# Kernel tuning notes

Hardware: AMD Instinct MI355X
Metric: run time of the kernel (lower is better)

## Reference

```python
import jax, jax.numpy as jnp
import numpy as np

B, N, DIN, DOUT, H = 4, 2048, 256, 256, 4
HD = DOUT // H
NEG_SLOPE = 0.2


def setup_inputs() -> dict:
    key = jax.random.key(0)
    k1, k2, k3, k4, k5 = jax.random.split(key, 5)
    x = jax.random.normal(k1, (B, N, DIN), dtype=jnp.float32)
    adj = jax.random.randint(k2, (B, N, N), 0, 2).astype(jnp.float32)
    # ensure self-loops so every softmax row has at least one valid entry
    adj = jnp.maximum(adj, jnp.eye(N, dtype=jnp.float32)[None])
    # xavier-uniform-ish scales
    w_bound = float(np.sqrt(6.0 / (DIN + DOUT)))
    a_bound = float(np.sqrt(6.0 / (1 + HD)))
    W = jax.random.uniform(k3, (DOUT, DIN), jnp.float32, -w_bound, w_bound)
    a_src = jax.random.uniform(k4, (H, HD), jnp.float32, -a_bound, a_bound)
    a_dst = jax.random.uniform(k5, (H, HD), jnp.float32, -a_bound, a_bound)
    return {"x": x, "adj": adj, "W": W, "a_src": a_src, "a_dst": a_dst}


def reference(x, adj, W, a_src, a_dst):
    b, n, _ = x.shape
    h = (x @ W.T).reshape(b, n, H, HD)                      # [B,N,H,HD]
    s_src = jnp.einsum('bnhd,hd->bnh', h, a_src)            # [B,N,H]
    s_dst = jnp.einsum('bnhd,hd->bnh', h, a_dst)            # [B,N,H]
    # e[b,i,j,h] = leaky_relu(s_src[b,i,h] + s_dst[b,j,h])
    e = jax.nn.leaky_relu(s_src[:, :, None, :] + s_dst[:, None, :, :], NEG_SLOPE)
    e = jnp.where(adj[..., None] == 0, -jnp.inf, e)         # [B,N,N,H]
    alpha = jax.nn.softmax(e, axis=2)                       # softmax over j (dropout is identity at eval)
    out = jnp.einsum('bijh,bjhd->bihd', alpha, h)           # weighted aggregate
    return out.reshape(b, n, DOUT)
```

## Files before the change

### kernel.cpp

```cpp
#include <hip/hip_runtime.h>
#include <math.h>

#define Bb   4
#define Nn   2048
#define Dd   256
#define Hh   4
#define HDd  64

typedef float v4f __attribute__((ext_vector_type(4)));
typedef short v8s __attribute__((ext_vector_type(8)));

__device__ __forceinline__ unsigned rne_bf16(float f) {
    unsigned u = __float_as_uint(f);
    u += 0x7fffu + ((u >> 16) & 1u);
    return u >> 16;
}

__global__ __launch_bounds__(256, 2) void k_gemm(const float* __restrict__ x,
                                                 const float* __restrict__ W,
                                                 const float* __restrict__ a_src,
                                                 const float* __restrict__ a_dst,
                                                 unsigned short* __restrict__ hbf,
                                                 float* __restrict__ ssrc,
                                                 float* __restrict__ sdst) {
    __shared__ __align__(16) unsigned short xs[2][64 * 72];
    __shared__ __align__(16) unsigned short wsm[2][64 * 72];
    __shared__ float asd[128];

    const int tid = threadIdx.x;
    const int m0 = (int)(blockIdx.x >> 2) * 64;
    const int head = (int)blockIdx.x & 3;
    const int n0 = head * 64;
    const int b = m0 >> 11;
    const int i0loc = m0 & 2047;

    if (tid < 128) {
        int sel = tid >> 6, d = tid & 63;
        asd[tid] = sel ? a_dst[n0 + d] : a_src[n0 + d];
    }

    const int wv = tid >> 6, ln = tid & 63, l15 = ln & 15, l4 = ln >> 4;
    const int mh = wv >> 1, nh = wv & 1;
    const int srow = tid >> 2, kq = (tid & 3) * 16;

    v4f acc[2][2];
#pragma unroll
    for (int g = 0; g < 2; ++g)
#pragma unroll
        for (int t = 0; t < 2; ++t) acc[g][t] = (v4f){0.f, 0.f, 0.f, 0.f};

    for (int st = 0; st < 4; ++st) {
        const int k0 = st * 64;
        __syncthreads();
        {
            float xf[16], wf[16];
            const float* xp = x + (size_t)(m0 + srow) * Dd + k0 + kq;
            const float* wp = W + (size_t)(n0 + srow) * Dd + k0 + kq;
#pragma unroll
            for (int q = 0; q < 4; ++q) {
                *(float4*)&xf[q * 4] = *(const float4*)(xp + q * 4);
                *(float4*)&wf[q * 4] = *(const float4*)(wp + q * 4);
            }
            unsigned xh[8], xl[8], wh[8], wl[8];
#pragma unroll
            for (int j = 0; j < 8; ++j) {
                unsigned h0 = rne_bf16(xf[2 * j]), h1 = rne_bf16(xf[2 * j + 1]);
                float l0 = xf[2 * j] - __uint_as_float(h0 << 16);
                float l1 = xf[2 * j + 1] - __uint_as_float(h1 << 16);
                xh[j] = h0 | (h1 << 16);
                xl[j] = rne_bf16(l0) | (rne_bf16(l1) << 16);
                unsigned g0 = rne_bf16(wf[2 * j]), g1 = rne_bf16(wf[2 * j + 1]);
                float m0f = wf[2 * j] - __uint_as_float(g0 << 16);
                float m1f = wf[2 * j + 1] - __uint_as_float(g1 << 16);
                wh[j] = g0 | (g1 << 16);
                wl[j] = rne_bf16(m0f) | (rne_bf16(m1f) << 16);
            }
            *(uint4*)(xs[0] + srow * 72 + kq)     = make_uint4(xh[0], xh[1], xh[2], xh[3]);
            *(uint4*)(xs[0] + srow * 72 + kq + 8) = make_uint4(xh[4], xh[5], xh[6], xh[7]);
            *(uint4*)(xs[1] + srow * 72 + kq)     = make_uint4(xl[0], xl[1], xl[2], xl[3]);
            *(uint4*)(xs[1] + srow * 72 + kq + 8) = make_uint4(xl[4], xl[5], xl[6], xl[7]);
            *(uint4*)(wsm[0] + srow * 72 + kq)     = make_uint4(wh[0], wh[1], wh[2], wh[3]);
            *(uint4*)(wsm[0] + srow * 72 + kq + 8) = make_uint4(wh[4], wh[5], wh[6], wh[7]);
            *(uint4*)(wsm[1] + srow * 72 + kq)     = make_uint4(wl[0], wl[1], wl[2], wl[3]);
            *(uint4*)(wsm[1] + srow * 72 + kq + 8) = make_uint4(wl[4], wl[5], wl[6], wl[7]);
        }
        __syncthreads();
        {
            v8s ah[2][2], al[2][2], bh_[2][2], bl_[2][2];
#pragma unroll
            for (int g = 0; g < 2; ++g)
#pragma unroll
                for (int kh = 0; kh < 2; ++kh) {
                    int ro = (mh * 32 + g * 16 + l15) * 72 + kh * 32 + l4 * 8;
                    ah[g][kh] = *(const v8s*)(xs[0] + ro);
                    al[g][kh] = *(const v8s*)(xs[1] + ro);
                }
#pragma unroll
            for (int t = 0; t < 2; ++t)
#pragma unroll
                for (int kh = 0; kh < 2; ++kh) {
                    int ro = (nh * 32 + t * 16 + l15) * 72 + kh * 32 + l4 * 8;
                    bh_[t][kh] = *(const v8s*)(wsm[0] + ro);
                    bl_[t][kh] = *(const v8s*)(wsm[1] + ro);
                }
#pragma unroll
            for (int g = 0; g < 2; ++g)
#pragma unroll
                for (int t = 0; t < 2; ++t)
#pragma unroll
                    for (int kh = 0; kh < 2; ++kh) {
                        acc[g][t] = __builtin_amdgcn_mfma_f32_16x16x32_bf16(ah[g][kh], bh_[t][kh], acc[g][t], 0, 0, 0);
                        acc[g][t] = __builtin_amdgcn_mfma_f32_16x16x32_bf16(al[g][kh], bh_[t][kh], acc[g][t], 0, 0, 0);
                        acc[g][t] = __builtin_amdgcn_mfma_f32_16x16x32_bf16(ah[g][kh], bl_[t][kh], acc[g][t], 0, 0, 0);
                    }
        }
    }

    __syncthreads();
    float* T = (float*)&xs[0][0];
#pragma unroll
    for (int g = 0; g < 2; ++g)
#pragma unroll
        for (int t = 0; t < 2; ++t)
#pragma unroll
            for (int r = 0; r < 4; ++r) {
                int d = nh * 32 + t * 16 + l15;
                int m = mh * 32 + g * 16 + l4 * 4 + r;
                T[d * 67 + m] = acc[g][t][r];
            }
    __syncthreads();
    if (tid < 128) {
        int m = tid & 63, sel = tid >> 6;
        float s = 0.f;
#pragma unroll
        for (int d = 0; d < 64; ++d) s += T[d * 67 + m] * asd[sel * 64 + d];
        (sel ? sdst : ssrc)[((size_t)b * Nn + i0loc + m) * Hh + head] = s;
        int dloc = tid >> 1, jh = tid & 1;
        const float* row = T + dloc * 67 + jh * 32;
        unsigned pk[16];
#pragma unroll
        for (int jj = 0; jj < 16; ++jj)
            pk[jj] = rne_bf16(row[jj * 2]) | (rne_bf16(row[jj * 2 + 1]) << 16);
        unsigned short* dst = hbf +
            ((size_t)((b * 64 + (i0loc >> 5) + jh) * 256 + head * HDd + dloc)) * 32;
        uint4* d4 = (uint4*)dst;
        d4[0] = make_uint4(pk[0], pk[1], pk[2], pk[3]);
        d4[1] = make_uint4(pk[4], pk[5], pk[6], pk[7]);
        d4[2] = make_uint4(pk[8], pk[9], pk[10], pk[11]);
        d4[3] = make_uint4(pk[12], pk[13], pk[14], pk[15]);
    }
}

__global__ __launch_bounds__(512, 4) void k_aggr(const unsigned short* __restrict__ hbf,
                                                 const float* __restrict__ adj,
                                                 const float* __restrict__ ssrc,
                                                 const float* __restrict__ sdst,
                                                 float* __restrict__ out) {
    __shared__ __align__(16) unsigned short Bh[128 * 72];
    __shared__ __align__(16) unsigned short Aw[64 * 72];

    const int tid = threadIdx.x;
    const int bid = (int)blockIdx.x;
    const int hp  = (bid >> 3) & 1;
    const int lin = (bid & 7) | ((bid >> 4) << 3);
    const int b  = lin >> 6;
    const int i0 = (lin & 63) * 32;

    const int gi = tid >> 4, jq = tid & 15;
    const int srow = tid >> 2, sseg = tid & 3;
    const int wv = tid >> 6;
    const int hl = wv >> 2, tl = wv & 3;
    const int ln = tid & 63, l15 = ln & 15, l4 = ln >> 4;

    const float2 s2 = *(const float2*)(ssrc + ((size_t)b * Nn + i0 + gi) * Hh + hp * 2);
    const float* adjr = adj + (size_t)b * Nn * Nn + (size_t)(i0 + gi) * Nn;
    const float* sdr = sdst + (size_t)b * Nn * Hh + hp * 2;

    const v8s ones = {0x3F80, 0x3F80, 0x3F80, 0x3F80, 0x3F80, 0x3F80, 0x3F80, 0x3F80};

    v4f acc[2], zac[2];
#pragma unroll
    for (int g = 0; g < 2; ++g) {
        acc[g] = (v4f){0.f, 0.f, 0.f, 0.f};
        zac[g] = (v4f){0.f, 0.f, 0.f, 0.f};
    }

    for (int st = 0; st < 32; ++st) {
        const int j0 = st * 64;
        const uint4* src = (const uint4*)(hbf +
            ((size_t)((b * 64 + 2 * st + (sseg >> 1)) * 256 + hp * 128 + srow)) * 32 +
            (sseg & 1) * 16);
        uint4 p0 = src[0], p1 = src[1];
        float4 ajv = *(const float4*)(adjr + j0 + jq * 4);
        float2 sd0 = *(const float2*)(sdr + (size_t)(j0 + jq * 4 + 0) * Hh);
        float2 sd1 = *(const float2*)(sdr + (size_t)(j0 + jq * 4 + 1) * Hh);
        float2 sd2 = *(const float2*)(sdr + (size_t)(j0 + jq * 4 + 2) * Hh);
        float2 sd3 = *(const float2*)(sdr + (size_t)(j0 + jq * 4 + 3) * Hh);
        __syncthreads();
        {
            uint4* dh = (uint4*)(Bh + srow * 72 + sseg * 16);
            dh[0] = p0; dh[1] = p1;
        }
        {
            const float adjv[4] = {ajv.x, ajv.y, ajv.z, ajv.w};
            const float2 sdv[4] = {sd0, sd1, sd2, sd3};
            unsigned pk0[2], pk1[2];
#pragma unroll
            for (int k = 0; k < 4; ++k) {
                float e0 = s2.x + sdv[k].x;
                float e1 = s2.y + sdv[k].y;
                e0 = fmaxf(e0, 0.2f * e0);
                e1 = fmaxf(e1, 0.2f * e1);
                unsigned u0 = rne_bf16(adjv[k] * __expf(e0));
                unsigned u1 = rne_bf16(adjv[k] * __expf(e1));
                if (k & 1) { pk0[k >> 1] |= u0 << 16; pk1[k >> 1] |= u1 << 16; }
                else       { pk0[k >> 1] = u0;        pk1[k >> 1] = u1; }
            }
            *(uint2*)(Aw + (gi) * 72 + jq * 4)      = make_uint2(pk0[0], pk0[1]);
            *(uint2*)(Aw + (32 + gi) * 72 + jq * 4) = make_uint2(pk1[0], pk1[1]);
        }
        __syncthreads();
        {
            v8s a[2][2], bf[2];
#pragma unroll
            for (int g = 0; g < 2; ++g)
#pragma unroll
                for (int kh = 0; kh < 2; ++kh)
                    a[g][kh] = *(const v8s*)(Aw + (hl * 32 + g * 16 + l15) * 72 + kh * 32 + l4 * 8);
#pragma unroll
            for (int kh = 0; kh < 2; ++kh)
                bf[kh] = *(const v8s*)(Bh + (hl * 64 + tl * 16 + l15) * 72 + kh * 32 + l4 * 8);
#pragma unroll
            for (int g = 0; g < 2; ++g)
#pragma unroll
                for (int kh = 0; kh < 2; ++kh) {
                    acc[g] = __builtin_amdgcn_mfma_f32_16x16x32_bf16(a[g][kh], bf[kh], acc[g], 0, 0, 0);
                    zac[g] = __builtin_amdgcn_mfma_f32_16x16x32_bf16(a[g][kh], ones, zac[g], 0, 0, 0);
                }
        }
    }

    const int head = hp * 2 + hl;
    const int d = head * HDd + tl * 16 + l15;
#pragma unroll
    for (int g = 0; g < 2; ++g)
#pragma unroll
        for (int r = 0; r < 4; ++r) {
            float zinv = 1.f / zac[g][r];
            int i = i0 + g * 16 + l4 * 4 + r;
            out[((size_t)b * Nn + i) * Dd + d] = acc[g][r] * zinv;
        }
}

extern "C" void kernel_launch(void* const* d_in, const int* in_sizes, int n_in,
                              void* d_out, int out_size, void* d_ws, size_t ws_size,
                              hipStream_t stream) {
    const float* x     = (const float*)d_in[0];
    const float* adj   = (const float*)d_in[1];
    const float* W     = (const float*)d_in[2];
    const float* a_src = (const float*)d_in[3];
    const float* a_dst = (const float*)d_in[4];
    float* out = (float*)d_out;

    unsigned short* hbf = (unsigned short*)d_ws;
    float* ssrc = (float*)(hbf + (size_t)Bb * Nn * Dd);
    float* sdst = ssrc + (size_t)Bb * Nn * Hh;

    k_gemm<<<dim3(512), dim3(256), 0, stream>>>(x, W, a_src, a_dst, hbf, ssrc, sdst);
    k_aggr<<<dim3(512), dim3(512), 0, stream>>>(hbf, adj, ssrc, sdst, out);
}
```

Baseline: 156.1 us.

## Double-buffer attention weights, load h directly to registers, transpose score layout

```diff
diff --git a/kernel.cpp b/kernel.cpp
--- a/kernel.cpp
+++ b/kernel.cpp
@@ -6,6 +6,7 @@
 #define Dd   256
 #define Hh   4
 #define HDd  64
+#define BN   (Bb * Nn)
 
 typedef float v4f __attribute__((ext_vector_type(4)));
 typedef short v8s __attribute__((ext_vector_type(8)));
@@ -134,7 +135,7 @@
         float s = 0.f;
 #pragma unroll
         for (int d = 0; d < 64; ++d) s += T[d * 67 + m] * asd[sel * 64 + d];
-        (sel ? sdst : ssrc)[((size_t)b * Nn + i0loc + m) * Hh + head] = s;
+        (sel ? sdst : ssrc)[(size_t)head * BN + (size_t)b * Nn + i0loc + m] = s;
         int dloc = tid >> 1, jh = tid & 1;
         const float* row = T + dloc * 67 + jh * 32;
         unsigned pk[16];
@@ -156,8 +157,7 @@
                                                  const float* __restrict__ ssrc,
                                                  const float* __restrict__ sdst,
                                                  float* __restrict__ out) {
-    __shared__ __align__(16) unsigned short Bh[128 * 72];
-    __shared__ __align__(16) unsigned short Aw[64 * 72];
+    __shared__ __align__(16) unsigned short Aw[2][64 * 72];
 
     const int tid = threadIdx.x;
     const int bid = (int)blockIdx.x;
@@ -167,14 +167,18 @@
     const int i0 = (lin & 63) * 32;
 
     const int gi = tid >> 4, jq = tid & 15;
-    const int srow = tid >> 2, sseg = tid & 3;
     const int wv = tid >> 6;
     const int hl = wv >> 2, tl = wv & 3;
     const int ln = tid & 63, l15 = ln & 15, l4 = ln >> 4;
 
-    const float2 s2 = *(const float2*)(ssrc + ((size_t)b * Nn + i0 + gi) * Hh + hp * 2);
+    const float ss0 = ssrc[(size_t)(hp * 2 + 0) * BN + (size_t)b * Nn + i0 + gi];
+    const float ss1 = ssrc[(size_t)(hp * 2 + 1) * BN + (size_t)b * Nn + i0 + gi];
     const float* adjr = adj + (size_t)b * Nn * Nn + (size_t)(i0 + gi) * Nn;
-    const float* sdr = sdst + (size_t)b * Nn * Hh + hp * 2;
+    const float* sdr0 = sdst + (size_t)(hp * 2 + 0) * BN + (size_t)b * Nn;
+    const float* sdr1 = sdst + (size_t)(hp * 2 + 1) * BN + (size_t)b * Nn;
+
+    const unsigned short* hrow = hbf +
+        ((size_t)b * 64 * 256 + (size_t)(hp * 128 + hl * 64 + tl * 16 + l15)) * 32 + l4 * 8;
 
     const v8s ones = {0x3F80, 0x3F80, 0x3F80, 0x3F80, 0x3F80, 0x3F80, 0x3F80, 0x3F80};
 
@@ -185,30 +189,20 @@
         zac[g] = (v4f){0.f, 0.f, 0.f, 0.f};
     }
 
+    float4 ajv = *(const float4*)(adjr + jq * 4);
+    float4 sda = *(const float4*)(sdr0 + jq * 4);
+    float4 sdb = *(const float4*)(sdr1 + jq * 4);
+
     for (int st = 0; st < 32; ++st) {
-        const int j0 = st * 64;
-        const uint4* src = (const uint4*)(hbf +
-            ((size_t)((b * 64 + 2 * st + (sseg >> 1)) * 256 + hp * 128 + srow)) * 32 +
-            (sseg & 1) * 16);
-        uint4 p0 = src[0], p1 = src[1];
-        float4 ajv = *(const float4*)(adjr + j0 + jq * 4);
-        float2 sd0 = *(const float2*)(sdr + (size_t)(j0 + jq * 4 + 0) * Hh);
-        float2 sd1 = *(const float2*)(sdr + (size_t)(j0 + jq * 4 + 1) * Hh);
-        float2 sd2 = *(const float2*)(sdr + (size_t)(j0 + jq * 4 + 2) * Hh);
-        float2 sd3 = *(const float2*)(sdr + (size_t)(j0 + jq * 4 + 3) * Hh);
-        __syncthreads();
-        {
-            uint4* dh = (uint4*)(Bh + srow * 72 + sseg * 16);
-            dh[0] = p0; dh[1] = p1;
-        }
         {
             const float adjv[4] = {ajv.x, ajv.y, ajv.z, ajv.w};
-            const float2 sdv[4] = {sd0, sd1, sd2, sd3};
+            const float sa[4] = {sda.x, sda.y, sda.z, sda.w};
+            const float sb[4] = {sdb.x, sdb.y, sdb.z, sdb.w};
             unsigned pk0[2], pk1[2];
 #pragma unroll
             for (int k = 0; k < 4; ++k) {
-                float e0 = s2.x + sdv[k].x;
-                float e1 = s2.y + sdv[k].y;
+                float e0 = ss0 + sa[k];
+                float e1 = ss1 + sb[k];
                 e0 = fmaxf(e0, 0.2f * e0);
                 e1 = fmaxf(e1, 0.2f * e1);
                 unsigned u0 = rne_bf16(adjv[k] * __expf(e0));
@@ -216,27 +210,32 @@
                 if (k & 1) { pk0[k >> 1] |= u0 << 16; pk1[k >> 1] |= u1 << 16; }
                 else       { pk0[k >> 1] = u0;        pk1[k >> 1] = u1; }
             }
-            *(uint2*)(Aw + (gi) * 72 + jq * 4)      = make_uint2(pk0[0], pk0[1]);
-            *(uint2*)(Aw + (32 + gi) * 72 + jq * 4) = make_uint2(pk1[0], pk1[1]);
+            *(uint2*)(Aw[st & 1] + gi * 72 + jq * 4)        = make_uint2(pk0[0], pk0[1]);
+            *(uint2*)(Aw[st & 1] + (32 + gi) * 72 + jq * 4) = make_uint2(pk1[0], pk1[1]);
         }
         __syncthreads();
         {
-            v8s a[2][2], bf[2];
-#pragma unroll
-            for (int g = 0; g < 2; ++g)
-#pragma unroll
-                for (int kh = 0; kh < 2; ++kh)
-                    a[g][kh] = *(const v8s*)(Aw + (hl * 32 + g * 16 + l15) * 72 + kh * 32 + l4 * 8);
-#pragma unroll
-            for (int kh = 0; kh < 2; ++kh)
-                bf[kh] = *(const v8s*)(Bh + (hl * 64 + tl * 16 + l15) * 72 + kh * 32 + l4 * 8);
-#pragma unroll
-            for (int g = 0; g < 2; ++g)
-#pragma unroll
-                for (int kh = 0; kh < 2; ++kh) {
-                    acc[g] = __builtin_amdgcn_mfma_f32_16x16x32_bf16(a[g][kh], bf[kh], acc[g], 0, 0, 0);
-                    zac[g] = __builtin_amdgcn_mfma_f32_16x16x32_bf16(a[g][kh], ones, zac[g], 0, 0, 0);
-                }
+            const int jn = ((st + 1) & 31) * 64;
+            ajv = *(const float4*)(adjr + jn + jq * 4);
+            sda = *(const float4*)(sdr0 + jn + jq * 4);
+            sdb = *(const float4*)(sdr1 + jn + jq * 4);
+        }
+        {
+            const unsigned short* awp = Aw[st & 1];
+            v8s b0 = *(const v8s*)(hrow + (size_t)(2 * st + 0) * 8192);
+            v8s b1 = *(const v8s*)(hrow + (size_t)(2 * st + 1) * 8192);
+            v8s a00 = *(const v8s*)(awp + (hl * 32 + l15) * 72 + l4 * 8);
+            v8s a01 = *(const v8s*)(awp + (hl * 32 + l15) * 72 + 32 + l4 * 8);
+            v8s a10 = *(const v8s*)(awp + (hl * 32 + 16 + l15) * 72 + l4 * 8);
+            v8s a11 = *(const v8s*)(awp + (hl * 32 + 16 + l15) * 72 + 32 + l4 * 8);
+            acc[0] = __builtin_amdgcn_mfma_f32_16x16x32_bf16(a00, b0, acc[0], 0, 0, 0);
+            acc[0] = __builtin_amdgcn_mfma_f32_16x16x32_bf16(a01, b1, acc[0], 0, 0, 0);
+            acc[1] = __builtin_amdgcn_mfma_f32_16x16x32_bf16(a10, b0, acc[1], 0, 0, 0);
+            acc[1] = __builtin_amdgcn_mfma_f32_16x16x32_bf16(a11, b1, acc[1], 0, 0, 0);
+            zac[0] = __builtin_amdgcn_mfma_f32_16x16x32_bf16(a00, ones, zac[0], 0, 0, 0);
+            zac[0] = __builtin_amdgcn_mfma_f32_16x16x32_bf16(a01, ones, zac[0], 0, 0, 0);
+            zac[1] = __builtin_amdgcn_mfma_f32_16x16x32_bf16(a10, ones, zac[1], 0, 0, 0);
+            zac[1] = __builtin_amdgcn_mfma_f32_16x16x32_bf16(a11, ones, zac[1], 0, 0, 0);
         }
     }
 
@@ -264,7 +263,7 @@
 
     unsigned short* hbf = (unsigned short*)d_ws;
     float* ssrc = (float*)(hbf + (size_t)Bb * Nn * Dd);
-    float* sdst = ssrc + (size_t)Bb * Nn * Hh;
+    float* sdst = ssrc + (size_t)Hh * BN;
 
     k_gemm<<<dim3(512), dim3(256), 0, stream>>>(x, W, a_src, a_dst, hbf, ssrc, sdst);
     k_aggr<<<dim3(512), dim3(512), 0, stream>>>(hbf, adj, ssrc, sdst, out);
```

After: 155.4 us. No clear change (-0.5%).
